# Kernel tuning notes

Measured on AMD Instinct MI355X. Metric: run time of the kernel, lower is better.

Reference implementation:

```python
import jax, jax.numpy as jnp
import numpy as np

BETA = 0.25


def setup_inputs() -> dict:
    key = jax.random.key(0)
    k1, k2 = jax.random.split(key)
    z_e = jax.random.normal(k1, (16, 256, 2048), dtype=jnp.float32)   # [B, C, L]
    # nn.Embedding weight initialized uniform(-1, 1): [num_codewords, codebook_dim]
    emb = jax.random.uniform(k2, (2048, 256), dtype=jnp.float32, minval=-1.0, maxval=1.0)
    return {"z_e": z_e, "emb": emb}


def reference(z_e, emb):
    C = emb.shape[1]
    # Faithful to the torch code: permute(2,1,0) -> [L, C, B], then view(-1, C)
    z = jnp.transpose(z_e, (2, 1, 0))          # [L, C, B]
    flat = z.reshape(-1, C)                    # [N, C] where N = L*C*B / C
    d = (jnp.sum(flat * flat, axis=1, keepdims=True)
         + jnp.sum(emb * emb, axis=1)
         - 2.0 * flat @ emb.T)                 # [N, K]
    indices = jnp.argmin(d, axis=1)            # [N]
    quantized = emb[indices].reshape(z.shape)  # [L, C, B]
    sg = jax.lax.stop_gradient
    vq_loss = (jnp.mean((sg(quantized) - z) ** 2)
               + BETA * jnp.mean((quantized - sg(z)) ** 2))
    return quantized, indices, vq_loss
```

## Files before the change

kernel.cpp:

```cpp
#include <hip/hip_runtime.h>


#define ZE_CL   (256 * 2048)
#define NROWS   32768
#define KC      2048
#define DD      256
#define IDX_OFF 8388608
#define LOSS_OFF (8388608 + 32768)
#define D2 8e-3f

typedef __bf16 bf16x4 __attribute__((ext_vector_type(4)));
typedef __bf16 bf16x8 __attribute__((ext_vector_type(8)));
typedef float  f32x4  __attribute__((ext_vector_type(4)));

#define EN_OFF  0u
#define EH_OFF  8192u
#define EL_OFF  (EH_OFF + 1048576u)
#define AH_OFF  (EL_OFF + 1048576u)
#define AL_OFF  (AH_OFF + 16777216u)
#define CNT_OFF (AL_OFF + 16777216u)
#define LST_OFF (CNT_OFF + 16u)
#define WS_NEED (LST_OFF + 131072u)

static __device__ inline void gld_lds16(const void* g, void* l) {
    __builtin_amdgcn_global_load_lds(
        (const __attribute__((address_space(1))) void*)g,
        (__attribute__((address_space(3))) void*)l, 16, 0, 0);
}

__global__ void vq_prep_emb(const float* __restrict__ emb, float* __restrict__ enorm,
                            __bf16* __restrict__ Eh, __bf16* __restrict__ El) {
    int tid = threadIdx.x;
    int col = blockIdx.x * 32 + (tid >> 3);
    int ch  = tid & 7;
    const float4* src = (const float4*)(emb + (size_t)col * DD);
    int t8 = col >> 8, g = (col >> 4) & 15, c = col & 15;
    float s = 0.f;
#pragma unroll
    for (int q = 0; q < 4; ++q) {
        float4 v0 = src[ch * 8 + q * 2];
        float4 v1 = src[ch * 8 + q * 2 + 1];
        float f[8] = {v0.x, v0.y, v0.z, v0.w, v1.x, v1.y, v1.z, v1.w};
        bf16x8 h, l;
#pragma unroll
        for (int j = 0; j < 8; ++j) {
            h[j] = (__bf16)f[j];
            l[j] = (__bf16)(f[j] - (float)h[j]);
            s += f[j] * f[j];
        }
        size_t off = ((size_t)(t8 * 8 + ch) * 16384) + (size_t)(g * 1024 + q * 256 + c * 16);
        *(bf16x8*)((char*)Eh + off) = h;
        *(bf16x8*)((char*)El + off) = l;
    }
    s += __shfl_xor(s, 1, 64);
    s += __shfl_xor(s, 2, 64);
    s += __shfl_xor(s, 4, 64);
    if (ch == 0) enorm[col] = s;
}

__global__ void vq_transpose_split(const float* __restrict__ ze, float* __restrict__ A,
                                   __bf16* __restrict__ Ah, __bf16* __restrict__ Al) {
    __shared__ float T[16 * 272];
    int tid = threadIdx.x;
    int m  = blockIdx.x & 15;
    int lt = blockIdx.x >> 4;
    int l0 = lt * 16;
#pragma unroll
    for (int it = 0; it < 4; ++it) {
        int p   = tid + it * 256;
        int b   = p >> 6;
        int clo = (p >> 2) & 15;
        int l4  = p & 3;
        const float* g = ze + (size_t)b * ZE_CL + (size_t)(m * 16 + clo) * 2048 + l0 + 4 * l4;
        float4 v = *(const float4*)g;
        int jp = 17 * clo + b;
        T[(4 * l4 + 0) * 272 + jp] = v.x;
        T[(4 * l4 + 1) * 272 + jp] = v.y;
        T[(4 * l4 + 2) * 272 + jp] = v.z;
        T[(4 * l4 + 3) * 272 + jp] = v.w;
    }
    __syncthreads();
#pragma unroll
    for (int it = 0; it < 4; ++it) {
        int p  = tid + it * 256;
        int ll = p >> 6;
        int c4 = p & 63;
        int j0 = 4 * c4;
        int base = ll * 272 + 17 * (j0 >> 4) + (j0 & 15);
        float4 v;
        v.x = T[base + 0]; v.y = T[base + 1]; v.z = T[base + 2]; v.w = T[base + 3];
        int n = (l0 + ll) * 16 + m;
        *(float4*)(A + (size_t)n * DD + j0) = v;
        if (Ah) {
            float a0 = -2.f * v.x, a1 = -2.f * v.y, a2 = -2.f * v.z, a3 = -2.f * v.w;
            bf16x4 h, l;
            h[0] = (__bf16)a0; l[0] = (__bf16)(a0 - (float)h[0]);
            h[1] = (__bf16)a1; l[1] = (__bf16)(a1 - (float)h[1]);
            h[2] = (__bf16)a2; l[2] = (__bf16)(a2 - (float)h[2]);
            h[3] = (__bf16)a3; l[3] = (__bf16)(a3 - (float)h[3]);
            int bn = n >> 6, mi = (n >> 4) & 3, r = n & 15;
            int ch = j0 >> 5, q = (j0 >> 3) & 3, hb = (j0 & 7) * 2;
            size_t off = (size_t)bn * 32768 + (size_t)((mi * 8 + ch) * 1024 + q * 256 + r * 16 + hb);
            *(bf16x4*)((char*)Ah + off) = h;
            *(bf16x4*)((char*)Al + off) = l;
        }
    }
}

__global__ __launch_bounds__(256, 2) void vq_main_mfma(
    const __bf16* __restrict__ Ah, const __bf16* __restrict__ Al,
    const __bf16* __restrict__ Eh, const __bf16* __restrict__ El,
    const float* __restrict__ enorm, const float* __restrict__ emb,
    float* out, int* __restrict__ rcount, int* __restrict__ rlist)
{
    __shared__ __align__(16) char sA[65536];
    __shared__ float sRv[256], sR2[256];
    __shared__ int   sRi[256];
    __shared__ int   sIdx[64], sFlag[64];
    __shared__ float wsum[4];

    const int tid  = threadIdx.x;
    const int wv   = tid >> 6;
    const int lane = tid & 63;
    const int l15  = lane & 15;
    const int n0   = blockIdx.x * 64;

    {
        const char* srcH = (const char*)Ah + (size_t)blockIdx.x * 32768;
        const char* srcL = (const char*)Al + (size_t)blockIdx.x * 32768;
#pragma unroll
        for (int it = 0; it < 8; ++it) {
            int off = (it * 4 + wv) * 1024;
            gld_lds16(srcH + off + lane * 16, sA + off);
            gld_lds16(srcL + off + lane * 16, sA + 32768 + off);
        }
    }

    const char* EhW = (const char*)Eh + (size_t)(wv * 4) * 1024 + (size_t)lane * 16;
    const char* ElW = (const char*)El + (size_t)(wv * 4) * 1024 + (size_t)lane * 16;
    const char* sAl16 = sA + (size_t)lane * 16;

    float v1[16], v2[16]; int i1[16];
#pragma unroll
    for (int s = 0; s < 16; ++s) { v1[s] = 3.4e38f; v2[s] = 3.4e38f; i1[s] = 0; }

    __syncthreads();

    for (int nt = 0; nt < 8; ++nt) {
        const char* EhT = EhW + (size_t)nt * 131072;
        const char* ElT = ElW + (size_t)nt * 131072;
        f32x4 acc[4][4];
#pragma unroll
        for (int a = 0; a < 4; ++a)
#pragma unroll
            for (int b = 0; b < 4; ++b) acc[a][b] = (f32x4){0.f, 0.f, 0.f, 0.f};

#pragma unroll 2
        for (int ch = 0; ch < 8; ++ch) {
            bf16x8 ah[4], al[4], bh[4], bl[4];
#pragma unroll
            for (int nj = 0; nj < 4; ++nj) {
                size_t boff = (size_t)(ch * 16384 + nj * 1024);
                bh[nj] = *(const bf16x8*)(EhT + boff);
                bl[nj] = *(const bf16x8*)(ElT + boff);
            }
#pragma unroll
            for (int mi = 0; mi < 4; ++mi) {
                size_t off = (size_t)((mi * 8 + ch) * 1024);
                ah[mi] = *(const bf16x8*)(sAl16 + off);
                al[mi] = *(const bf16x8*)(sAl16 + 32768 + off);
            }
#pragma unroll
            for (int mi = 0; mi < 4; ++mi)
#pragma unroll
                for (int nj = 0; nj < 4; ++nj)
                    acc[mi][nj] = __builtin_amdgcn_mfma_f32_16x16x32_bf16(ah[mi], bh[nj], acc[mi][nj], 0, 0, 0);
#pragma unroll
            for (int mi = 0; mi < 4; ++mi)
#pragma unroll
                for (int nj = 0; nj < 4; ++nj)
                    acc[mi][nj] = __builtin_amdgcn_mfma_f32_16x16x32_bf16(ah[mi], bl[nj], acc[mi][nj], 0, 0, 0);
#pragma unroll
            for (int mi = 0; mi < 4; ++mi)
#pragma unroll
                for (int nj = 0; nj < 4; ++nj)
                    acc[mi][nj] = __builtin_amdgcn_mfma_f32_16x16x32_bf16(al[mi], bh[nj], acc[mi][nj], 0, 0, 0);
        }
#pragma unroll
        for (int nj = 0; nj < 4; ++nj) {
            int k = nt * 256 + wv * 64 + nj * 16 + l15;
            float en = enorm[k];
#pragma unroll
            for (int mi = 0; mi < 4; ++mi)
#pragma unroll
                for (int r = 0; r < 4; ++r) {
                    float d = acc[mi][nj][r] + en;
                    int slot = mi * 4 + r;
                    float nv2 = fminf(v2[slot], fmaxf(v1[slot], d));
                    if (d < v1[slot]) i1[slot] = k;
                    v1[slot] = fminf(v1[slot], d);
                    v2[slot] = nv2;
                }
        }
    }

    const int quad = lane >> 4;
#pragma unroll
    for (int slot = 0; slot < 16; ++slot) {
        float a1 = v1[slot], a2 = v2[slot];
        int ai = i1[slot];
#pragma unroll
        for (int m = 1; m < 16; m <<= 1) {
            float b1 = __shfl_xor(a1, m, 64);
            float b2 = __shfl_xor(a2, m, 64);
            int bi = __shfl_xor(ai, m, 64);
            float n2 = fminf(fminf(a2, b2), fmaxf(a1, b1));
            if (b1 < a1) ai = bi;
            a1 = fminf(a1, b1);
            a2 = n2;
        }
        if (l15 == 0) {
            int row = (slot >> 2) * 16 + quad * 4 + (slot & 3);
            sRv[row * 4 + wv] = a1;
            sR2[row * 4 + wv] = a2;
            sRi[row * 4 + wv] = ai;
        }
    }
    __syncthreads();
    if (tid < 64) {
        float a1 = sRv[tid * 4], a2 = sR2[tid * 4];
        int ai = sRi[tid * 4];
#pragma unroll
        for (int w2 = 1; w2 < 4; ++w2) {
            float b1 = sRv[tid * 4 + w2], b2 = sR2[tid * 4 + w2];
            int bi = sRi[tid * 4 + w2];
            float n2 = fminf(fminf(a2, b2), fmaxf(a1, b1));
            if (b1 < a1) ai = bi;
            a1 = fminf(a1, b1);
            a2 = n2;
        }
        int fg = (a2 - a1 < D2) ? 1 : 0;
        sIdx[tid] = ai;
        sFlag[tid] = fg;
        out[IDX_OFF + n0 + tid] = (float)ai;
        if (fg) { int p = atomicAdd(rcount, 1); rlist[p] = n0 + tid; }
    }
    __syncthreads();

    float lacc = 0.f;
#pragma unroll
    for (int it = 0; it < 16; ++it) {
        int p = tid + it * 256;
        int r = p >> 6;
        int c4 = p & 63;
        if (!sFlag[r]) {
            int k = sIdx[r];
            size_t off = (size_t)(n0 + r) * DD + 4 * c4;
            float4 q = *(const float4*)(emb + (size_t)k * DD + 4 * c4);
            float4 a = *(const float4*)(out + off);
            float dx = q.x - a.x, dy = q.y - a.y, dz = q.z - a.z, dw = q.w - a.w;
            lacc += dx * dx + dy * dy + dz * dz + dw * dw;
            *(float4*)(out + off) = q;
        }
    }
#pragma unroll
    for (int off = 32; off > 0; off >>= 1) lacc += __shfl_down(lacc, off, 64);
    if ((tid & 63) == 0) wsum[tid >> 6] = lacc;
    __syncthreads();
    if (tid == 0) {
        float bs = wsum[0] + wsum[1] + wsum[2] + wsum[3];
        atomicAdd(out + LOSS_OFF, bs * (1.25f / 8388608.0f));
    }
}

__global__ void vq_rescore(const float* __restrict__ emb, const float* __restrict__ enorm,
                           float* out, const int* __restrict__ rcount,
                           const int* __restrict__ rlist) {
    __shared__ float sX[256];
    __shared__ float sV[256];
    __shared__ int   sK[256];
    __shared__ float sP[256];
    int cnt = *rcount;
    int tid = threadIdx.x;
    for (int li = blockIdx.x; li < cnt; li += gridDim.x) {
        int row = rlist[li];
        __syncthreads();
        sX[tid] = out[(size_t)row * DD + tid];
        __syncthreads();
        float bv = 3.4e38f; int bk = 0;
        for (int jj = 0; jj < 8; ++jj) {
            int k = jj * 256 + tid;
            const float4* e4 = (const float4*)(emb + (size_t)k * DD);
            float dot = 0.f;
#pragma unroll 8
            for (int d4 = 0; d4 < 64; ++d4) {
                float4 e = e4[d4];
                float4 x = *(const float4*)(sX + d4 * 4);
                dot += x.x * e.x + x.y * e.y + x.z * e.z + x.w * e.w;
            }
            float s = enorm[k] - 2.f * dot;
            if (s < bv) { bv = s; bk = k; }
        }
        sV[tid] = bv; sK[tid] = bk;
        __syncthreads();
#pragma unroll
        for (int s = 128; s > 0; s >>= 1) {
            if (tid < s) {
                float vo = sV[tid + s]; int ko = sK[tid + s];
                if (vo < sV[tid] || (vo == sV[tid] && ko < sK[tid])) { sV[tid] = vo; sK[tid] = ko; }
            }
            __syncthreads();
        }
        int k = sK[0];
        float x = sX[tid];
        float q = emb[(size_t)k * DD + tid];
        out[(size_t)row * DD + tid] = q;
        float d = q - x;
        sP[tid] = d * d;
        __syncthreads();
#pragma unroll
        for (int s = 128; s > 0; s >>= 1) {
            if (tid < s) sP[tid] += sP[tid + s];
            __syncthreads();
        }
        if (tid == 0) {
            out[IDX_OFF + row] = (float)k;
            atomicAdd(out + LOSS_OFF, sP[0] * (1.25f / 8388608.0f));
        }
    }
}

__global__ __launch_bounds__(256, 2) void vq_main_f32(const float* __restrict__ emb,
                                                      const float* __restrict__ enorm,
                                                      float* out) {
    const int SA = 68, SE = 68;
    __shared__ float smem[64 * 68 + 64 * 68];
    __shared__ int   sIdx[64];
    __shared__ float wsum[4];
    float* sA = smem;
    float* sEb = smem + 64 * SA;
    float* redv = sEb;
    int*   redi = (int*)(sEb + 64 * 16);
    int tid = threadIdx.x;
    int n0 = blockIdx.x * 64;
    int rg = tid & 15;
    int kg = tid >> 4;
    float minv[4]; int mini[4];
#pragma unroll
    for (int i = 0; i < 4; ++i) { minv[i] = 3.4e38f; mini[i] = 0; }
    const float* A = out;
    for (int kt = 0; kt < KC / 64; ++kt) {
        int k0 = kt * 64;
        float acc[4][4];
#pragma unroll
        for (int i = 0; i < 4; ++i)
#pragma unroll
            for (int j = 0; j < 4; ++j) acc[i][j] = 0.f;
        for (int dc = 0; dc < 4; ++dc) {
            int d0 = dc * 64;
            __syncthreads();
#pragma unroll
            for (int it = 0; it < 4; ++it) {
                int p = tid + it * 256, r = p >> 4, c4 = p & 15;
                *(float4*)(sA + r * SA + 4 * c4) =
                    *(const float4*)(A + (size_t)(n0 + r) * DD + d0 + 4 * c4);
            }
#pragma unroll
            for (int it = 0; it < 4; ++it) {
                int p = tid + it * 256, r = p >> 4, c4 = p & 15;
                *(float4*)(sEb + r * SE + 4 * c4) =
                    *(const float4*)(emb + (size_t)(k0 + r) * DD + d0 + 4 * c4);
            }
            __syncthreads();
#pragma unroll
            for (int d4 = 0; d4 < 16; ++d4) {
                float4 av[4], ev[4];
#pragma unroll
                for (int i = 0; i < 4; ++i) av[i] = *(const float4*)(sA + (rg + 16 * i) * SA + 4 * d4);
#pragma unroll
                for (int j = 0; j < 4; ++j) ev[j] = *(const float4*)(sEb + (kg + 16 * j) * SE + 4 * d4);
#pragma unroll
                for (int i = 0; i < 4; ++i)
#pragma unroll
                    for (int j = 0; j < 4; ++j)
                        acc[i][j] += av[i].x * ev[j].x + av[i].y * ev[j].y +
                                     av[i].z * ev[j].z + av[i].w * ev[j].w;
            }
        }
#pragma unroll
        for (int j = 0; j < 4; ++j) {
            int k = k0 + kg + 16 * j;
            float en = enorm[k];
#pragma unroll
            for (int i = 0; i < 4; ++i) {
                float s = en - 2.f * acc[i][j];
                if (s < minv[i]) { minv[i] = s; mini[i] = k; }
            }
        }
    }
    __syncthreads();
#pragma unroll
    for (int i = 0; i < 4; ++i) {
        int r = rg + 16 * i;
        redv[r * 16 + kg] = minv[i];
        redi[r * 16 + kg] = mini[i];
    }
    __syncthreads();
    if (tid < 64) {
        float bv = redv[tid * 16]; int bi = redi[tid * 16];
        for (int t = 1; t < 16; ++t) {
            float v = redv[tid * 16 + t]; int ii = redi[tid * 16 + t];
            if (v < bv || (v == bv && ii < bi)) { bv = v; bi = ii; }
        }
        sIdx[tid] = bi;
        out[IDX_OFF + n0 + tid] = (float)bi;
    }
    __syncthreads();
    float lacc = 0.f;
#pragma unroll
    for (int it = 0; it < 16; ++it) {
        int p = tid + it * 256, r = p >> 6, c4 = p & 63;
        int k = sIdx[r];
        size_t off = (size_t)(n0 + r) * DD + 4 * c4;
        float4 q = *(const float4*)(emb + (size_t)k * DD + 4 * c4);
        float4 a = *(const float4*)(out + off);
        float dx = q.x - a.x, dy = q.y - a.y, dz = q.z - a.z, dw = q.w - a.w;
        lacc += dx * dx + dy * dy + dz * dz + dw * dw;
        *(float4*)(out + off) = q;
    }
#pragma unroll
    for (int off = 32; off > 0; off >>= 1) lacc += __shfl_down(lacc, off, 64);
    if ((tid & 63) == 0) wsum[tid >> 6] = lacc;
    __syncthreads();
    if (tid == 0) {
        float bs = wsum[0] + wsum[1] + wsum[2] + wsum[3];
        atomicAdd(out + LOSS_OFF, bs * (1.25f / 8388608.0f));
    }
}

extern "C" void kernel_launch(void* const* d_in, const int* in_sizes, int n_in,
                              void* d_out, int out_size, void* d_ws, size_t ws_size,
                              hipStream_t stream) {
    (void)in_sizes; (void)n_in; (void)out_size;
    const float* ze  = (const float*)d_in[0];
    const float* emb = (const float*)d_in[1];
    float* out = (float*)d_out;
    char*  ws  = (char*)d_ws;
    float* enorm = (float*)(ws + EN_OFF);

    hipMemsetAsync((char*)d_out + (size_t)LOSS_OFF * 4, 0, 4, stream);

    if (ws_size >= (size_t)WS_NEED) {
        __bf16* Eh = (__bf16*)(ws + EH_OFF);
        __bf16* El = (__bf16*)(ws + EL_OFF);
        __bf16* Ah = (__bf16*)(ws + AH_OFF);
        __bf16* Al = (__bf16*)(ws + AL_OFF);
        int* rcount = (int*)(ws + CNT_OFF);
        int* rlist  = (int*)(ws + LST_OFF);
        hipMemsetAsync(ws + CNT_OFF, 0, 16, stream);
        vq_prep_emb<<<64, 256, 0, stream>>>(emb, enorm, Eh, El);
        vq_transpose_split<<<2048, 256, 0, stream>>>(ze, out, Ah, Al);
        vq_main_mfma<<<NROWS / 64, 256, 0, stream>>>(Ah, Al, Eh, El, enorm, emb, out, rcount, rlist);
        vq_rescore<<<64, 256, 0, stream>>>(emb, enorm, out, rcount, rlist);
    } else {
        vq_prep_emb<<<64, 256, 0, stream>>>(emb, enorm, (__bf16*)(ws + EH_OFF), (__bf16*)(ws + EH_OFF));
        vq_transpose_split<<<2048, 256, 0, stream>>>(ze, out, (__bf16*)0, (__bf16*)0);
        vq_main_f32<<<NROWS / 64, 256, 0, stream>>>(emb, enorm, out);
    }
}
```

Measured before the change: 275.2 us.

## Fuse prep kernels and memsets, halve main-kernel row tile to 32

Merges the embedding-prep and transpose/split kernels into one launch, with extra blocks that also zero the loss and rescore counters, so the memsets and one launch disappear. The MFMA main kernel now processes 32 rows per block instead of 64, doubling the grid to 1024 blocks and halving LDS and register use per block. The rescore grid grows from 64 to 512 blocks. The smaller tile re-reads the codebook twice as often per row in exchange for better occupancy and load balance across CUs.

```diff
diff --git a/kernel.cpp b/kernel.cpp
--- a/kernel.cpp
+++ b/kernel.cpp
@@ -28,42 +28,52 @@
         (__attribute__((address_space(3))) void*)l, 16, 0, 0);
 }
 
-__global__ void vq_prep_emb(const float* __restrict__ emb, float* __restrict__ enorm,
-                            __bf16* __restrict__ Eh, __bf16* __restrict__ El) {
-    int tid = threadIdx.x;
-    int col = blockIdx.x * 32 + (tid >> 3);
-    int ch  = tid & 7;
-    const float4* src = (const float4*)(emb + (size_t)col * DD);
-    int t8 = col >> 8, g = (col >> 4) & 15, c = col & 15;
-    float s = 0.f;
-#pragma unroll
-    for (int q = 0; q < 4; ++q) {
-        float4 v0 = src[ch * 8 + q * 2];
-        float4 v1 = src[ch * 8 + q * 2 + 1];
-        float f[8] = {v0.x, v0.y, v0.z, v0.w, v1.x, v1.y, v1.z, v1.w};
-        bf16x8 h, l;
-#pragma unroll
-        for (int j = 0; j < 8; ++j) {
-            h[j] = (__bf16)f[j];
-            l[j] = (__bf16)(f[j] - (float)h[j]);
-            s += f[j] * f[j];
-        }
-        size_t off = ((size_t)(t8 * 8 + ch) * 16384) + (size_t)(g * 1024 + q * 256 + c * 16);
-        *(bf16x8*)((char*)Eh + off) = h;
-        *(bf16x8*)((char*)El + off) = l;
-    }
-    s += __shfl_xor(s, 1, 64);
-    s += __shfl_xor(s, 2, 64);
-    s += __shfl_xor(s, 4, 64);
-    if (ch == 0) enorm[col] = s;
-}
-
-__global__ void vq_transpose_split(const float* __restrict__ ze, float* __restrict__ A,
-                                   __bf16* __restrict__ Ah, __bf16* __restrict__ Al) {
+__global__ void vq_prep_all(const float* __restrict__ ze, const float* __restrict__ emb,
+                            float* __restrict__ out, float* __restrict__ enorm,
+                            __bf16* __restrict__ Eh, __bf16* __restrict__ El,
+                            __bf16* __restrict__ Ah, __bf16* __restrict__ Al,
+                            int* __restrict__ rcount) {
     __shared__ float T[16 * 272];
     int tid = threadIdx.x;
-    int m  = blockIdx.x & 15;
-    int lt = blockIdx.x >> 4;
+    int bid = blockIdx.x;
+
+    if (bid >= 2048) {
+        int pb = bid - 2048;
+        if (pb == 0) {
+            if (tid < 4) rcount[tid] = 0;
+            if (tid == 4) out[LOSS_OFF] = 0.f;
+        }
+        int col = pb * 32 + (tid >> 3);
+        int ch  = tid & 7;
+        const float4* src = (const float4*)(emb + (size_t)col * DD);
+        int t8 = col >> 8, g = (col >> 4) & 15, c = col & 15;
+        float s = 0.f;
+#pragma unroll
+        for (int q = 0; q < 4; ++q) {
+            float4 v0 = src[ch * 8 + q * 2];
+            float4 v1 = src[ch * 8 + q * 2 + 1];
+            float f[8] = {v0.x, v0.y, v0.z, v0.w, v1.x, v1.y, v1.z, v1.w};
+            bf16x8 h, l;
+#pragma unroll
+            for (int j = 0; j < 8; ++j) {
+                h[j] = (__bf16)f[j];
+                l[j] = (__bf16)(f[j] - (float)h[j]);
+                s += f[j] * f[j];
+            }
+            size_t off = ((size_t)(t8 * 8 + ch) * 16384) + (size_t)(g * 1024 + q * 256 + c * 16);
+            *(bf16x8*)((char*)Eh + off) = h;
+            *(bf16x8*)((char*)El + off) = l;
+        }
+        s += __shfl_xor(s, 1, 64);
+        s += __shfl_xor(s, 2, 64);
+        s += __shfl_xor(s, 4, 64);
+        if (ch == 0) enorm[col] = s;
+        return;
+    }
+
+    float* A = out;
+    int m  = bid & 15;
+    int lt = bid >> 4;
     int l0 = lt * 16;
 #pragma unroll
     for (int it = 0; it < 4; ++it) {
@@ -91,7 +101,7 @@
         v.x = T[base + 0]; v.y = T[base + 1]; v.z = T[base + 2]; v.w = T[base + 3];
         int n = (l0 + ll) * 16 + m;
         *(float4*)(A + (size_t)n * DD + j0) = v;
-        if (Ah) {
+        {
             float a0 = -2.f * v.x, a1 = -2.f * v.y, a2 = -2.f * v.z, a3 = -2.f * v.w;
             bf16x4 h, l;
             h[0] = (__bf16)a0; l[0] = (__bf16)(a0 - (float)h[0]);
@@ -113,26 +123,29 @@
     const float* __restrict__ enorm, const float* __restrict__ emb,
     float* out, int* __restrict__ rcount, int* __restrict__ rlist)
 {
-    __shared__ __align__(16) char sA[65536];
-    __shared__ float sRv[256], sR2[256];
-    __shared__ int   sRi[256];
-    __shared__ int   sIdx[64], sFlag[64];
+    __shared__ __align__(16) char sA[32768];
+    __shared__ float sRv[128], sR2[128];
+    __shared__ int   sRi[128];
+    __shared__ int   sIdx[32], sFlag[32];
     __shared__ float wsum[4];
 
     const int tid  = threadIdx.x;
     const int wv   = tid >> 6;
     const int lane = tid & 63;
     const int l15  = lane & 15;
-    const int n0   = blockIdx.x * 64;
+    const int quad = lane >> 4;
+    const int n0   = blockIdx.x * 32;
+    const int bn   = blockIdx.x >> 1;
+    const int miB  = (blockIdx.x & 1) * 2;
 
     {
-        const char* srcH = (const char*)Ah + (size_t)blockIdx.x * 32768;
-        const char* srcL = (const char*)Al + (size_t)blockIdx.x * 32768;
-#pragma unroll
-        for (int it = 0; it < 8; ++it) {
+        const char* srcH = (const char*)Ah + (size_t)bn * 32768 + (size_t)miB * 8192;
+        const char* srcL = (const char*)Al + (size_t)bn * 32768 + (size_t)miB * 8192;
+#pragma unroll
+        for (int it = 0; it < 4; ++it) {
             int off = (it * 4 + wv) * 1024;
             gld_lds16(srcH + off + lane * 16, sA + off);
-            gld_lds16(srcL + off + lane * 16, sA + 32768 + off);
+            gld_lds16(srcL + off + lane * 16, sA + 16384 + off);
         }
     }
 
@@ -140,24 +153,24 @@
     const char* ElW = (const char*)El + (size_t)(wv * 4) * 1024 + (size_t)lane * 16;
     const char* sAl16 = sA + (size_t)lane * 16;
 
-    float v1[16], v2[16]; int i1[16];
-#pragma unroll
-    for (int s = 0; s < 16; ++s) { v1[s] = 3.4e38f; v2[s] = 3.4e38f; i1[s] = 0; }
+    float v1[8], v2[8]; int i1[8];
+#pragma unroll
+    for (int s = 0; s < 8; ++s) { v1[s] = 3.4e38f; v2[s] = 3.4e38f; i1[s] = 0; }
 
     __syncthreads();
 
     for (int nt = 0; nt < 8; ++nt) {
         const char* EhT = EhW + (size_t)nt * 131072;
         const char* ElT = ElW + (size_t)nt * 131072;
-        f32x4 acc[4][4];
-#pragma unroll
-        for (int a = 0; a < 4; ++a)
+        f32x4 acc[2][4];
+#pragma unroll
+        for (int a = 0; a < 2; ++a)
 #pragma unroll
             for (int b = 0; b < 4; ++b) acc[a][b] = (f32x4){0.f, 0.f, 0.f, 0.f};
 
 #pragma unroll 2
         for (int ch = 0; ch < 8; ++ch) {
-            bf16x8 ah[4], al[4], bh[4], bl[4];
+            bf16x8 ah[2], al[2], bh[4], bl[4];
 #pragma unroll
             for (int nj = 0; nj < 4; ++nj) {
                 size_t boff = (size_t)(ch * 16384 + nj * 1024);
@@ -165,23 +178,23 @@
                 bl[nj] = *(const bf16x8*)(ElT + boff);
             }
 #pragma unroll
-            for (int mi = 0; mi < 4; ++mi) {
+            for (int mi = 0; mi < 2; ++mi) {
                 size_t off = (size_t)((mi * 8 + ch) * 1024);
                 ah[mi] = *(const bf16x8*)(sAl16 + off);
-                al[mi] = *(const bf16x8*)(sAl16 + 32768 + off);
-            }
-#pragma unroll
-            for (int mi = 0; mi < 4; ++mi)
+                al[mi] = *(const bf16x8*)(sAl16 + 16384 + off);
+            }
+#pragma unroll
+            for (int mi = 0; mi < 2; ++mi)
 #pragma unroll
                 for (int nj = 0; nj < 4; ++nj)
                     acc[mi][nj] = __builtin_amdgcn_mfma_f32_16x16x32_bf16(ah[mi], bh[nj], acc[mi][nj], 0, 0, 0);
 #pragma unroll
-            for (int mi = 0; mi < 4; ++mi)
+            for (int mi = 0; mi < 2; ++mi)
 #pragma unroll
                 for (int nj = 0; nj < 4; ++nj)
                     acc[mi][nj] = __builtin_amdgcn_mfma_f32_16x16x32_bf16(ah[mi], bl[nj], acc[mi][nj], 0, 0, 0);
 #pragma unroll
-            for (int mi = 0; mi < 4; ++mi)
+            for (int mi = 0; mi < 2; ++mi)
 #pragma unroll
                 for (int nj = 0; nj < 4; ++nj)
                     acc[mi][nj] = __builtin_amdgcn_mfma_f32_16x16x32_bf16(al[mi], bh[nj], acc[mi][nj], 0, 0, 0);
@@ -191,7 +204,7 @@
             int k = nt * 256 + wv * 64 + nj * 16 + l15;
             float en = enorm[k];
 #pragma unroll
-            for (int mi = 0; mi < 4; ++mi)
+            for (int mi = 0; mi < 2; ++mi)
 #pragma unroll
                 for (int r = 0; r < 4; ++r) {
                     float d = acc[mi][nj][r] + en;
@@ -204,9 +217,8 @@
         }
     }
 
-    const int quad = lane >> 4;
-#pragma unroll
-    for (int slot = 0; slot < 16; ++slot) {
+#pragma unroll
+    for (int slot = 0; slot < 8; ++slot) {
         float a1 = v1[slot], a2 = v2[slot];
         int ai = i1[slot];
 #pragma unroll
@@ -227,7 +239,7 @@
         }
     }
     __syncthreads();
-    if (tid < 64) {
+    if (tid < 32) {
         float a1 = sRv[tid * 4], a2 = sR2[tid * 4];
         int ai = sRi[tid * 4];
 #pragma unroll
@@ -249,7 +261,7 @@
 
     float lacc = 0.f;
 #pragma unroll
-    for (int it = 0; it < 16; ++it) {
+    for (int it = 0; it < 8; ++it) {
         int p = tid + it * 256;
         int r = p >> 6;
         int c4 = p & 63;
@@ -330,6 +342,85 @@
     }
 }
 
+__global__ void vq_prep_emb(const float* __restrict__ emb, float* __restrict__ enorm,
+                            __bf16* __restrict__ Eh, __bf16* __restrict__ El) {
+    int tid = threadIdx.x;
+    int col = blockIdx.x * 32 + (tid >> 3);
+    int ch  = tid & 7;
+    const float4* src = (const float4*)(emb + (size_t)col * DD);
+    int t8 = col >> 8, g = (col >> 4) & 15, c = col & 15;
+    float s = 0.f;
+#pragma unroll
+    for (int q = 0; q < 4; ++q) {
+        float4 v0 = src[ch * 8 + q * 2];
+        float4 v1 = src[ch * 8 + q * 2 + 1];
+        float f[8] = {v0.x, v0.y, v0.z, v0.w, v1.x, v1.y, v1.z, v1.w};
+        bf16x8 h, l;
+#pragma unroll
+        for (int j = 0; j < 8; ++j) {
+            h[j] = (__bf16)f[j];
+            l[j] = (__bf16)(f[j] - (float)h[j]);
+            s += f[j] * f[j];
+        }
+        size_t off = ((size_t)(t8 * 8 + ch) * 16384) + (size_t)(g * 1024 + q * 256 + c * 16);
+        *(bf16x8*)((char*)Eh + off) = h;
+        *(bf16x8*)((char*)El + off) = l;
+    }
+    s += __shfl_xor(s, 1, 64);
+    s += __shfl_xor(s, 2, 64);
+    s += __shfl_xor(s, 4, 64);
+    if (ch == 0) enorm[col] = s;
+}
+
+__global__ void vq_transpose_split(const float* __restrict__ ze, float* __restrict__ A,
+                                   __bf16* __restrict__ Ah, __bf16* __restrict__ Al) {
+    __shared__ float T[16 * 272];
+    int tid = threadIdx.x;
+    int m  = blockIdx.x & 15;
+    int lt = blockIdx.x >> 4;
+    int l0 = lt * 16;
+#pragma unroll
+    for (int it = 0; it < 4; ++it) {
+        int p   = tid + it * 256;
+        int b   = p >> 6;
+        int clo = (p >> 2) & 15;
+        int l4  = p & 3;
+        const float* g = ze + (size_t)b * ZE_CL + (size_t)(m * 16 + clo) * 2048 + l0 + 4 * l4;
+        float4 v = *(const float4*)g;
+        int jp = 17 * clo + b;
+        T[(4 * l4 + 0) * 272 + jp] = v.x;
+        T[(4 * l4 + 1) * 272 + jp] = v.y;
+        T[(4 * l4 + 2) * 272 + jp] = v.z;
+        T[(4 * l4 + 3) * 272 + jp] = v.w;
+    }
+    __syncthreads();
+#pragma unroll
+    for (int it = 0; it < 4; ++it) {
+        int p  = tid + it * 256;
+        int ll = p >> 6;
+        int c4 = p & 63;
+        int j0 = 4 * c4;
+        int base = ll * 272 + 17 * (j0 >> 4) + (j0 & 15);
+        float4 v;
+        v.x = T[base + 0]; v.y = T[base + 1]; v.z = T[base + 2]; v.w = T[base + 3];
+        int n = (l0 + ll) * 16 + m;
+        *(float4*)(A + (size_t)n * DD + j0) = v;
+        if (Ah) {
+            float a0 = -2.f * v.x, a1 = -2.f * v.y, a2 = -2.f * v.z, a3 = -2.f * v.w;
+            bf16x4 h, l;
+            h[0] = (__bf16)a0; l[0] = (__bf16)(a0 - (float)h[0]);
+            h[1] = (__bf16)a1; l[1] = (__bf16)(a1 - (float)h[1]);
+            h[2] = (__bf16)a2; l[2] = (__bf16)(a2 - (float)h[2]);
+            h[3] = (__bf16)a3; l[3] = (__bf16)(a3 - (float)h[3]);
+            int bn = n >> 6, mi = (n >> 4) & 3, r = n & 15;
+            int ch = j0 >> 5, q = (j0 >> 3) & 3, hb = (j0 & 7) * 2;
+            size_t off = (size_t)bn * 32768 + (size_t)((mi * 8 + ch) * 1024 + q * 256 + r * 16 + hb);
+            *(bf16x4*)((char*)Ah + off) = h;
+            *(bf16x4*)((char*)Al + off) = l;
+        }
+    }
+}
+
 __global__ __launch_bounds__(256, 2) void vq_main_f32(const float* __restrict__ emb,
                                                       const float* __restrict__ enorm,
                                                       float* out) {
@@ -448,8 +539,6 @@
     char*  ws  = (char*)d_ws;
     float* enorm = (float*)(ws + EN_OFF);
 
-    hipMemsetAsync((char*)d_out + (size_t)LOSS_OFF * 4, 0, 4, stream);
-
     if (ws_size >= (size_t)WS_NEED) {
         __bf16* Eh = (__bf16*)(ws + EH_OFF);
         __bf16* El = (__bf16*)(ws + EL_OFF);
@@ -457,12 +546,11 @@
         __bf16* Al = (__bf16*)(ws + AL_OFF);
         int* rcount = (int*)(ws + CNT_OFF);
         int* rlist  = (int*)(ws + LST_OFF);
-        hipMemsetAsync(ws + CNT_OFF, 0, 16, stream);
-        vq_prep_emb<<<64, 256, 0, stream>>>(emb, enorm, Eh, El);
-        vq_transpose_split<<<2048, 256, 0, stream>>>(ze, out, Ah, Al);
-        vq_main_mfma<<<NROWS / 64, 256, 0, stream>>>(Ah, Al, Eh, El, enorm, emb, out, rcount, rlist);
-        vq_rescore<<<64, 256, 0, stream>>>(emb, enorm, out, rcount, rlist);
+        vq_prep_all<<<2112, 256, 0, stream>>>(ze, emb, out, enorm, Eh, El, Ah, Al, rcount);
+        vq_main_mfma<<<NROWS / 32, 256, 0, stream>>>(Ah, Al, Eh, El, enorm, emb, out, rcount, rlist);
+        vq_rescore<<<512, 256, 0, stream>>>(emb, enorm, out, rcount, rlist);
     } else {
+        hipMemsetAsync((char*)d_out + (size_t)LOSS_OFF * 4, 0, 4, stream);
         vq_prep_emb<<<64, 256, 0, stream>>>(emb, enorm, (__bf16*)(ws + EH_OFF), (__bf16*)(ws + EH_OFF));
         vq_transpose_split<<<2048, 256, 0, stream>>>(ze, out, (__bf16*)0, (__bf16*)0);
         vq_main_f32<<<NROWS / 64, 256, 0, stream>>>(emb, enorm, out);
```

After: 277.7 us. Within noise of the previous version (+0.9%).
